# Kernel optimization log

Measured on AMD Instinct MI355X. Metric: run time of the kernel, lower is better.

Reference implementation:

```python
import jax, jax.numpy as jnp
import numpy as np

EPS = 1e-12  # matches torch F.normalize default eps
SCALE = 64.0  # fixed softmax temperature from the source

def _l2_normalize(x, axis):
    n = jnp.linalg.norm(x, ord=2, axis=axis, keepdims=True)
    return x / jnp.maximum(n, EPS)

def setup_inputs() -> dict:
    key = jax.random.key(0)
    k1, k2, k3 = jax.random.split(key, 3)
    B, L, S, D = 8, 2048, 2048, 128
    return {
        "query": jax.random.normal(k1, (B, L, D), dtype=jnp.float32),
        "key": jax.random.normal(k2, (B, S, D), dtype=jnp.float32),
        "value": jax.random.normal(k3, (B, S, D), dtype=jnp.float32),
    }

def reference(query, key, value):
    # rank-3 query path with norm=True, return_value=True, return_score=False
    q = _l2_normalize(query, axis=2)   # [B, L, D]
    k = _l2_normalize(key, axis=2)     # [B, S, D]
    score = jnp.einsum('nlk,nsk->nls', q, k)            # [B, L, S]
    score = jax.nn.softmax(score * SCALE, axis=2)
    # original does broadcast-multiply-then-sum; equivalent contraction:
    out = jnp.einsum('nls,nsd->nld', score, value)      # [B, L, D]
    return out
```

## Files before the change

### kernel.cpp

```cpp
#include <hip/hip_runtime.h>
#include <stdint.h>

#define Bb 8
#define Ll 2048
#define Ss 2048
#define Dd 128
#define NSB 4
#define SCHUNK 512
#define NROWS 16384
#define SCALE_LOG2E 92.33248261689366f

typedef __attribute__((ext_vector_type(8))) short bf16x8;
typedef __attribute__((ext_vector_type(16))) float f32x16;
typedef __attribute__((ext_vector_type(4))) unsigned u32x4;

__device__ __forceinline__ unsigned f2bf_pack(float a, float b) {
  unsigned ua = __float_as_uint(a); ua += 0x7fffu + ((ua >> 16) & 1u);
  unsigned ub = __float_as_uint(b); ub += 0x7fffu + ((ub >> 16) & 1u);
  return (ua >> 16) | (ub & 0xffff0000u);
}

__device__ __forceinline__ unsigned pkbf(float a, float b) {
#if __has_builtin(__builtin_amdgcn_cvt_pk_bf16_f32)
  auto r = __builtin_amdgcn_cvt_pk_bf16_f32(a, b);
  return __builtin_bit_cast(unsigned, r);
#else
  return f2bf_pack(a, b);
#endif
}

__device__ __forceinline__ void gl_lds16(const void* g, void* l) {
  __builtin_amdgcn_global_load_lds(
      (const __attribute__((address_space(1))) unsigned*)g,
      (__attribute__((address_space(3))) unsigned*)l, 16, 0, 0);
}

#define TRS 138
extern "C" __global__ __launch_bounds__(256)
void prep_kern(const float* __restrict__ Q, const float* __restrict__ K,
               const float* __restrict__ V,
               unsigned short* __restrict__ Qn, unsigned short* __restrict__ Kn,
               unsigned short* __restrict__ Vt) {
  __shared__ unsigned short T[32 * TRS];
  const int t = threadIdx.x;
  const int bid = blockIdx.x;
  if (bid < 8192) {
    const int lane = t & 63;
    int row = (bid << 2) + (t >> 6);
    int r = row;
    const float* src = Q; unsigned short* dst = Qn;
    if (row >= NROWS) { r = row - NROWS; src = K; dst = Kn; }
    float2 f = *(const float2*)(src + (size_t)r * Dd + lane * 2);
    float ss = f.x * f.x + f.y * f.y;
#pragma unroll
    for (int m = 1; m < 64; m <<= 1) ss += __shfl_xor(ss, m, 64);
    float inv = 1.0f / fmaxf(sqrtf(ss), 1e-12f);
    *(unsigned*)(dst + (size_t)r * Dd + lane * 2) = pkbf(f.x * inv, f.y * inv);
  } else {
    const int vb = bid - 8192;
    const int b = vb & 7, sw = vb >> 3;
    const int d4 = t & 31, sr = t >> 5;
#pragma unroll
    for (int p = 0; p < 4; ++p) {
      int sl = p * 8 + sr;
      float4 v = *(const float4*)(V + ((size_t)(b * Ss + sw * 32 + sl)) * Dd + d4 * 4);
      *(unsigned*)&T[sl * TRS + d4 * 4]     = pkbf(v.x, v.y);
      *(unsigned*)&T[sl * TRS + d4 * 4 + 2] = pkbf(v.z, v.w);
    }
    __syncthreads();
    const int so = t & 3, db = t >> 2;
#pragma unroll
    for (int p = 0; p < 2; ++p) {
      int d = p * 64 + db;
      unsigned u[4];
#pragma unroll
      for (int k = 0; k < 4; ++k) {
        unsigned lo = T[(so * 8 + 2 * k) * TRS + d];
        unsigned hi = T[(so * 8 + 2 * k + 1) * TRS + d];
        u[k] = lo | (hi << 16);
      }
      *(uint4*)(Vt + ((size_t)(b * Dd + d)) * Ss + sw * 32 + so * 8) =
          make_uint4(u[0], u[1], u[2], u[3]);
    }
  }
}

extern "C" __global__ __launch_bounds__(256, 2)
void attn_kern(const unsigned short* __restrict__ Qn,
               const unsigned short* __restrict__ Kn,
               const unsigned short* __restrict__ Vt,
               unsigned short* __restrict__ Op,
               float* __restrict__ Lp) {
  __shared__ unsigned short Kl[2][16 * 512];
  __shared__ unsigned short Vl[2][16 * 512];
  const int tid = threadIdx.x, wv = tid >> 6, lane = tid & 63;
  const int lm = lane & 31, h = lane >> 5;
  const int gid = blockIdx.x;
  const int grp = gid & 31, qt = gid >> 5;
  const int b = grp >> 2, sb = grp & 3;
  const int sbase = sb * SCHUNK;
  const int qrow = qt * 128 + wv * 32 + lm;

  const unsigned short* Qrow = Qn + ((size_t)(b * Ll + qrow)) * Dd;
  bf16x8 qf[8];
#pragma unroll
  for (int kt = 0; kt < 8; ++kt)
    qf[kt] = *(const bf16x8*)(Qrow + kt * 16 + h * 8);

  const unsigned short* Kb = Kn + (size_t)b * Ss * Dd;
  const unsigned short* Vb = Vt + (size_t)b * Dd * Ss;

  f32x16 o[4];
#pragma unroll
  for (int i = 0; i < 4; ++i)
#pragma unroll
    for (int r = 0; r < 16; ++r) o[i][r] = 0.f;

  auto stage = [&](int it, int buf) {
    const int s0 = sbase + it * 64;
#pragma unroll
    for (int i = 0; i < 4; ++i) {
      const int ks = wv * 4 + i;
      gl_lds16(Kb + (size_t)(s0 + (ks >> 3) * 32 + lm) * Dd + (ks & 7) * 16 + h * 8,
               &Kl[buf][ks * 512]);
    }
#pragma unroll
    for (int i = 0; i < 4; ++i) {
      const int vs = wv * 4 + i;
      gl_lds16(Vb + (size_t)((vs >> 2) * 32 + lm) * Ss + s0 + (vs & 3) * 16 + h * 8,
               &Vl[buf][vs * 512]);
    }
  };
  stage(0, 0);

  float lrun = 0.f;

#pragma unroll 1
  for (int it = 0; it < 8; ++it) {
    __syncthreads();
    const int cur = it & 1;
    if (it + 1 < 8) stage(it + 1, cur ^ 1);

    f32x16 st[2];
#pragma unroll
    for (int sblk = 0; sblk < 2; ++sblk) {
      f32x16 acc;
#pragma unroll
      for (int r = 0; r < 16; ++r) acc[r] = 0.f;
#pragma unroll
      for (int kt = 0; kt < 8; ++kt) {
        bf16x8 kf = *(const bf16x8*)&Kl[cur][(sblk * 8 + kt) * 512 + lane * 8];
        acc = __builtin_amdgcn_mfma_f32_32x32x16_bf16(kf, qf[kt], acc, 0, 0, 0);
      }
      st[sblk] = acc;
    }

    float ls = 0.f;
#pragma unroll
    for (int t = 0; t < 4; ++t) {
      float p[8];
#pragma unroll
      for (int j = 0; j < 8; ++j)
        p[j] = __builtin_amdgcn_exp2f(
            __builtin_fmaf(st[t >> 1][(t & 1) * 8 + j], SCALE_LOG2E, -SCALE_LOG2E));
      ls += ((p[0] + p[1]) + (p[2] + p[3])) + ((p[4] + p[5]) + (p[6] + p[7]));
      unsigned u0 = pkbf(p[0], p[1]), u1 = pkbf(p[2], p[3]);
      unsigned u2 = pkbf(p[4], p[5]), u3 = pkbf(p[6], p[7]);
      unsigned s0 = (unsigned)__shfl_xor((int)u0, 32, 64);
      unsigned s1 = (unsigned)__shfl_xor((int)u1, 32, 64);
      unsigned s2 = (unsigned)__shfl_xor((int)u2, 32, 64);
      unsigned s3 = (unsigned)__shfl_xor((int)u3, 32, 64);
      u32x4 fr;
      fr.x = h ? s2 : u0;
      fr.y = h ? s3 : u1;
      fr.z = h ? u2 : s0;
      fr.w = h ? u3 : s1;
      bf16x8 pf = __builtin_bit_cast(bf16x8, fr);
#pragma unroll
      for (int dblk = 0; dblk < 4; ++dblk) {
        bf16x8 vf = *(const bf16x8*)&Vl[cur][(dblk * 4 + t) * 512 + lane * 8];
        o[dblk] = __builtin_amdgcn_mfma_f32_32x32x16_bf16(vf, pf, o[dblk], 0, 0, 0);
      }
    }
    lrun += ls;
  }

  const float lt = lrun + __shfl_xor(lrun, 32, 64);
  unsigned short* Ob = Op + ((size_t)sb * NROWS + b * Ll + qrow) * Dd;
#pragma unroll
  for (int dblk = 0; dblk < 4; ++dblk)
#pragma unroll
    for (int g = 0; g < 4; ++g) {
      uint2 w;
      w.x = pkbf(o[dblk][g * 4 + 0], o[dblk][g * 4 + 1]);
      w.y = pkbf(o[dblk][g * 4 + 2], o[dblk][g * 4 + 3]);
      *(uint2*)(Ob + dblk * 32 + g * 8 + h * 4) = w;
    }
  if (h == 0) Lp[sb * NROWS + b * Ll + qrow] = lt;
}

extern "C" __global__ __launch_bounds__(256)
void comb_kern(const unsigned short* __restrict__ Op,
               const float* __restrict__ Lp, float* __restrict__ Out) {
  const int idx = blockIdx.x * 256 + threadIdx.x;
  const int row = idx >> 5;
  const int dof = (idx & 31) * 4;
  float den = 0.f;
#pragma unroll
  for (int s = 0; s < NSB; ++s) den += Lp[s * NROWS + row];
  float a0 = 0.f, a1 = 0.f, a2 = 0.f, a3 = 0.f;
#pragma unroll
  for (int s = 0; s < NSB; ++s) {
    uint2 v = *(const uint2*)(Op + ((size_t)s * NROWS + row) * Dd + dof);
    a0 += __uint_as_float(v.x << 16);
    a1 += __uint_as_float(v.x & 0xffff0000u);
    a2 += __uint_as_float(v.y << 16);
    a3 += __uint_as_float(v.y & 0xffff0000u);
  }
  const float inv = 1.f / den;
  float4 r; r.x = a0 * inv; r.y = a1 * inv; r.z = a2 * inv; r.w = a3 * inv;
  *(float4*)(Out + (size_t)row * Dd + dof) = r;
}

extern "C" void kernel_launch(void* const* d_in, const int* in_sizes, int n_in,
                              void* d_out, int out_size, void* d_ws, size_t ws_size,
                              hipStream_t stream) {
  const float* Q = (const float*)d_in[0];
  const float* K = (const float*)d_in[1];
  const float* V = (const float*)d_in[2];
  float* Out = (float*)d_out;
  unsigned short* Qn = (unsigned short*)d_ws;
  unsigned short* Kn = Qn + (size_t)NROWS * Dd;
  unsigned short* Vt = Kn + (size_t)NROWS * Dd;
  unsigned short* Op = Vt + (size_t)Bb * Dd * Ss;
  float* Lp = (float*)(Op + (size_t)NSB * NROWS * Dd);
  hipLaunchKernelGGL(prep_kern, dim3(8192 + 512), dim3(256), 0, stream, Q, K, V, Qn, Kn, Vt);
  hipLaunchKernelGGL(attn_kern, dim3(512), dim3(256), 0, stream, Qn, Kn, Vt, Op, Lp);
  hipLaunchKernelGGL(comb_kern, dim3(2048), dim3(256), 0, stream, Op, Lp, Out);
}
```

Before: 110.8 us.

## Split keys into eight chunks, load V directly to registers, shrink LDS

The key dimension is now split into eight 256-wide chunks instead of four, which doubles the attention grid to 1024 blocks. Each iteration now covers 32 keys instead of 64. V fragments are loaded straight from global memory into registers instead of being staged through LDS, so LDS holds only a double-buffered K tile and occupancy can rise to three blocks per CU. In exchange, the combine kernel must read twice as many bf16 partial outputs and the partial-output workspace doubles. The direct V loads are not covered by the pipeline, so their latency may be exposed.

After: 144.4 us. 1.3x slower.

```diff
diff --git a/kernel.cpp b/kernel.cpp
--- a/kernel.cpp
+++ b/kernel.cpp
@@ -5,8 +5,8 @@
 #define Ll 2048
 #define Ss 2048
 #define Dd 128
-#define NSB 4
-#define SCHUNK 512
+#define NSB 8
+#define SCHUNK 256
 #define NROWS 16384
 #define SCALE_LOG2E 92.33248261689366f
 
@@ -85,19 +85,18 @@
   }
 }
 
-extern "C" __global__ __launch_bounds__(256, 2)
+extern "C" __global__ __launch_bounds__(256, 3)
 void attn_kern(const unsigned short* __restrict__ Qn,
                const unsigned short* __restrict__ Kn,
                const unsigned short* __restrict__ Vt,
                unsigned short* __restrict__ Op,
                float* __restrict__ Lp) {
-  __shared__ unsigned short Kl[2][16 * 512];
-  __shared__ unsigned short Vl[2][16 * 512];
+  __shared__ unsigned short Kl[2][8 * 512];
   const int tid = threadIdx.x, wv = tid >> 6, lane = tid & 63;
   const int lm = lane & 31, h = lane >> 5;
   const int gid = blockIdx.x;
-  const int grp = gid & 31, qt = gid >> 5;
-  const int b = grp >> 2, sb = grp & 3;
+  const int grp = gid & 63, qt = gid >> 6;
+  const int b = grp >> 3, sb = grp & 7;
   const int sbase = sb * SCHUNK;
   const int qrow = qt * 128 + wv * 32 + lm;
 
@@ -116,22 +115,15 @@
 #pragma unroll
     for (int r = 0; r < 16; ++r) o[i][r] = 0.f;
 
-  auto stage = [&](int it, int buf) {
-    const int s0 = sbase + it * 64;
-#pragma unroll
-    for (int i = 0; i < 4; ++i) {
-      const int ks = wv * 4 + i;
-      gl_lds16(Kb + (size_t)(s0 + (ks >> 3) * 32 + lm) * Dd + (ks & 7) * 16 + h * 8,
-               &Kl[buf][ks * 512]);
-    }
-#pragma unroll
-    for (int i = 0; i < 4; ++i) {
-      const int vs = wv * 4 + i;
-      gl_lds16(Vb + (size_t)((vs >> 2) * 32 + lm) * Ss + s0 + (vs & 3) * 16 + h * 8,
-               &Vl[buf][vs * 512]);
+  auto stageK = [&](int it, int buf) {
+    const int s0 = sbase + it * 32;
+#pragma unroll
+    for (int i = 0; i < 2; ++i) {
+      const int kt = wv * 2 + i;
+      gl_lds16(Kb + (size_t)(s0 + lm) * Dd + kt * 16 + h * 8, &Kl[buf][kt * 512]);
     }
   };
-  stage(0, 0);
+  stageK(0, 0);
 
   float lrun = 0.f;
 
@@ -139,46 +131,49 @@
   for (int it = 0; it < 8; ++it) {
     __syncthreads();
     const int cur = it & 1;
-    if (it + 1 < 8) stage(it + 1, cur ^ 1);
-
-    f32x16 st[2];
-#pragma unroll
-    for (int sblk = 0; sblk < 2; ++sblk) {
-      f32x16 acc;
-#pragma unroll
-      for (int r = 0; r < 16; ++r) acc[r] = 0.f;
-#pragma unroll
-      for (int kt = 0; kt < 8; ++kt) {
-        bf16x8 kf = *(const bf16x8*)&Kl[cur][(sblk * 8 + kt) * 512 + lane * 8];
-        acc = __builtin_amdgcn_mfma_f32_32x32x16_bf16(kf, qf[kt], acc, 0, 0, 0);
-      }
-      st[sblk] = acc;
+    const int s0 = sbase + it * 32;
+    uint4 vfr[8];
+#pragma unroll
+    for (int dblk = 0; dblk < 4; ++dblk)
+#pragma unroll
+      for (int t = 0; t < 2; ++t)
+        vfr[dblk * 2 + t] =
+            *(const uint4*)(Vb + (size_t)(dblk * 32 + lm) * Ss + s0 + t * 16 + h * 8);
+    if (it + 1 < 8) stageK(it + 1, cur ^ 1);
+
+    f32x16 acc;
+#pragma unroll
+    for (int r = 0; r < 16; ++r) acc[r] = 0.f;
+#pragma unroll
+    for (int kt = 0; kt < 8; ++kt) {
+      bf16x8 kf = *(const bf16x8*)&Kl[cur][kt * 512 + lane * 8];
+      acc = __builtin_amdgcn_mfma_f32_32x32x16_bf16(kf, qf[kt], acc, 0, 0, 0);
     }
 
     float ls = 0.f;
 #pragma unroll
-    for (int t = 0; t < 4; ++t) {
+    for (int t = 0; t < 2; ++t) {
       float p[8];
 #pragma unroll
       for (int j = 0; j < 8; ++j)
         p[j] = __builtin_amdgcn_exp2f(
-            __builtin_fmaf(st[t >> 1][(t & 1) * 8 + j], SCALE_LOG2E, -SCALE_LOG2E));
+            __builtin_fmaf(acc[t * 8 + j], SCALE_LOG2E, -SCALE_LOG2E));
       ls += ((p[0] + p[1]) + (p[2] + p[3])) + ((p[4] + p[5]) + (p[6] + p[7]));
       unsigned u0 = pkbf(p[0], p[1]), u1 = pkbf(p[2], p[3]);
       unsigned u2 = pkbf(p[4], p[5]), u3 = pkbf(p[6], p[7]);
-      unsigned s0 = (unsigned)__shfl_xor((int)u0, 32, 64);
-      unsigned s1 = (unsigned)__shfl_xor((int)u1, 32, 64);
-      unsigned s2 = (unsigned)__shfl_xor((int)u2, 32, 64);
-      unsigned s3 = (unsigned)__shfl_xor((int)u3, 32, 64);
+      unsigned s0p = (unsigned)__shfl_xor((int)u0, 32, 64);
+      unsigned s1p = (unsigned)__shfl_xor((int)u1, 32, 64);
+      unsigned s2p = (unsigned)__shfl_xor((int)u2, 32, 64);
+      unsigned s3p = (unsigned)__shfl_xor((int)u3, 32, 64);
       u32x4 fr;
-      fr.x = h ? s2 : u0;
-      fr.y = h ? s3 : u1;
-      fr.z = h ? u2 : s0;
-      fr.w = h ? u3 : s1;
+      fr.x = h ? s2p : u0;
+      fr.y = h ? s3p : u1;
+      fr.z = h ? u2 : s0p;
+      fr.w = h ? u3 : s1p;
       bf16x8 pf = __builtin_bit_cast(bf16x8, fr);
 #pragma unroll
       for (int dblk = 0; dblk < 4; ++dblk) {
-        bf16x8 vf = *(const bf16x8*)&Vl[cur][(dblk * 4 + t) * 512 + lane * 8];
+        bf16x8 vf = __builtin_bit_cast(bf16x8, vfr[dblk * 2 + t]);
         o[dblk] = __builtin_amdgcn_mfma_f32_32x32x16_bf16(vf, pf, o[dblk], 0, 0, 0);
       }
     }
@@ -235,6 +230,6 @@
   unsigned short* Op = Vt + (size_t)Bb * Dd * Ss;
   float* Lp = (float*)(Op + (size_t)NSB * NROWS * Dd);
   hipLaunchKernelGGL(prep_kern, dim3(8192 + 512), dim3(256), 0, stream, Q, K, V, Qn, Kn, Vt);
-  hipLaunchKernelGGL(attn_kern, dim3(512), dim3(256), 0, stream, Qn, Kn, Vt, Op, Lp);
+  hipLaunchKernelGGL(attn_kern, dim3(1024), dim3(256), 0, stream, Qn, Kn, Vt, Op, Lp);
   hipLaunchKernelGGL(comb_kern, dim3(2048), dim3(256), 0, stream, Op, Lp, Out);
 }
```

## Pre-swizzle K and V into MFMA fragment order to remove shuffles

Applied to the files above, without the earlier changes.

The prep kernel now writes normalized K and transposed V directly in the per-lane MFMA fragment layout, as contiguous 4096-element tiles per 32-row block. The attention kernel then stages them with fully contiguous global-to-LDS loads. It also reorders V so the P fragment can be packed without cross-half-wave shuffles, and fuses the softmax/PV step into the QK loop. This aims to cut strided global loads and the ds_swizzle/select overhead, at the cost of a more complex prep kernel with an LDS round trip for K.

Measured after the change: 107.2 us. 1.03x faster.

```diff
diff --git a/kernel.cpp b/kernel.cpp
--- a/kernel.cpp
+++ b/kernel.cpp
@@ -12,7 +12,6 @@
 
 typedef __attribute__((ext_vector_type(8))) short bf16x8;
 typedef __attribute__((ext_vector_type(16))) float f32x16;
-typedef __attribute__((ext_vector_type(4))) unsigned u32x4;
 
 __device__ __forceinline__ unsigned f2bf_pack(float a, float b) {
   unsigned ua = __float_as_uint(a); ua += 0x7fffu + ((ua >> 16) & 1u);
@@ -35,60 +34,101 @@
       (__attribute__((address_space(3))) unsigned*)l, 16, 0, 0);
 }
 
-#define TRS 138
+
 extern "C" __global__ __launch_bounds__(256)
 void prep_kern(const float* __restrict__ Q, const float* __restrict__ K,
                const float* __restrict__ V,
-               unsigned short* __restrict__ Qn, unsigned short* __restrict__ Kn,
-               unsigned short* __restrict__ Vt) {
-  __shared__ unsigned short T[32 * TRS];
+               unsigned short* __restrict__ Qn, unsigned short* __restrict__ Kf,
+               unsigned short* __restrict__ Vf) {
+  __shared__ float Tf[32 * 130];
+  __shared__ float Ps[32 * 8];
+  __shared__ float Nr[32];
+  __shared__ unsigned short Tb[32 * 128];
   const int t = threadIdx.x;
   const int bid = blockIdx.x;
-  if (bid < 8192) {
+  if (bid < 4096) {
     const int lane = t & 63;
-    int row = (bid << 2) + (t >> 6);
-    int r = row;
-    const float* src = Q; unsigned short* dst = Qn;
-    if (row >= NROWS) { r = row - NROWS; src = K; dst = Kn; }
-    float2 f = *(const float2*)(src + (size_t)r * Dd + lane * 2);
+    const int r = bid * 4 + (t >> 6);
+    float2 f = *(const float2*)(Q + (size_t)r * Dd + lane * 2);
     float ss = f.x * f.x + f.y * f.y;
 #pragma unroll
     for (int m = 1; m < 64; m <<= 1) ss += __shfl_xor(ss, m, 64);
     float inv = 1.0f / fmaxf(sqrtf(ss), 1e-12f);
-    *(unsigned*)(dst + (size_t)r * Dd + lane * 2) = pkbf(f.x * inv, f.y * inv);
+    *(unsigned*)(Qn + (size_t)r * Dd + lane * 2) = pkbf(f.x * inv, f.y * inv);
+  } else if (bid < 4608) {
+    const int kb = bid - 4096;
+    const int b = kb & 7, sw = kb >> 3;
+    const int sl = t >> 3, d0 = (t & 7) * 16;
+    const float* src = K + ((size_t)(b * Ss + sw * 32 + sl)) * Dd + d0;
+    float ss = 0.f;
+#pragma unroll
+    for (int i = 0; i < 4; ++i) {
+      float4 v = *(const float4*)(src + i * 4);
+      Tf[sl * 130 + d0 + i * 4 + 0] = v.x;
+      Tf[sl * 130 + d0 + i * 4 + 1] = v.y;
+      Tf[sl * 130 + d0 + i * 4 + 2] = v.z;
+      Tf[sl * 130 + d0 + i * 4 + 3] = v.w;
+      ss += v.x * v.x + v.y * v.y + v.z * v.z + v.w * v.w;
+    }
+    Ps[sl * 8 + (t & 7)] = ss;
+    __syncthreads();
+    if (t < 32) {
+      float s = 0.f;
+#pragma unroll
+      for (int j = 0; j < 8; ++j) s += Ps[t * 8 + j];
+      Nr[t] = 1.0f / fmaxf(sqrtf(s), 1e-12f);
+    }
+    __syncthreads();
+    unsigned short* Ko = Kf + ((size_t)(b * 64 + sw)) * 4096;
+#pragma unroll
+    for (int p = 0; p < 2; ++p) {
+      const int run = p * 256 + t;
+      const int lane = run & 63, s = lane & 31, h = lane >> 5;
+      const int d = (run >> 6) * 16 + h * 8;
+      const float n = Nr[s];
+      const float* row = &Tf[s * 130 + d];
+      uint4 w;
+      w.x = pkbf(row[0] * n, row[1] * n);
+      w.y = pkbf(row[2] * n, row[3] * n);
+      w.z = pkbf(row[4] * n, row[5] * n);
+      w.w = pkbf(row[6] * n, row[7] * n);
+      *(uint4*)(Ko + run * 8) = w;
+    }
   } else {
-    const int vb = bid - 8192;
+    const int vb = bid - 4608;
     const int b = vb & 7, sw = vb >> 3;
-    const int d4 = t & 31, sr = t >> 5;
-#pragma unroll
-    for (int p = 0; p < 4; ++p) {
-      int sl = p * 8 + sr;
-      float4 v = *(const float4*)(V + ((size_t)(b * Ss + sw * 32 + sl)) * Dd + d4 * 4);
-      *(unsigned*)&T[sl * TRS + d4 * 4]     = pkbf(v.x, v.y);
-      *(unsigned*)&T[sl * TRS + d4 * 4 + 2] = pkbf(v.z, v.w);
-    }
-    __syncthreads();
-    const int so = t & 3, db = t >> 2;
+    const int sl = t >> 3, d0 = (t & 7) * 16;
+    const float* src = V + ((size_t)(b * Ss + sw * 32 + sl)) * Dd + d0;
+#pragma unroll
+    for (int i = 0; i < 4; ++i) {
+      float4 v = *(const float4*)(src + i * 4);
+      *(unsigned*)&Tb[sl * 128 + d0 + i * 4]     = pkbf(v.x, v.y);
+      *(unsigned*)&Tb[sl * 128 + d0 + i * 4 + 2] = pkbf(v.z, v.w);
+    }
+    __syncthreads();
+    unsigned short* Vo = Vf + ((size_t)(b * 64 + sw)) * 4096;
 #pragma unroll
     for (int p = 0; p < 2; ++p) {
-      int d = p * 64 + db;
-      unsigned u[4];
-#pragma unroll
-      for (int k = 0; k < 4; ++k) {
-        unsigned lo = T[(so * 8 + 2 * k) * TRS + d];
-        unsigned hi = T[(so * 8 + 2 * k + 1) * TRS + d];
-        u[k] = lo | (hi << 16);
+      const int run = p * 256 + t;
+      const int vslot = run >> 6, lane = run & 63;
+      const int dloc = lane & 31, h = lane >> 5;
+      const int dblk = vslot >> 1, t2 = vslot & 1;
+      const int d = dblk * 32 + dloc;
+      unsigned short w[8];
+#pragma unroll
+      for (int j = 0; j < 8; ++j) {
+        const int sloc = t2 * 16 + 4 * h + (j & 3) + 8 * (j >> 2);
+        w[j] = Tb[sloc * 128 + d];
       }
-      *(uint4*)(Vt + ((size_t)(b * Dd + d)) * Ss + sw * 32 + so * 8) =
-          make_uint4(u[0], u[1], u[2], u[3]);
+      *(uint4*)(Vo + run * 8) = *(uint4*)w;
     }
   }
 }
 
 extern "C" __global__ __launch_bounds__(256, 2)
 void attn_kern(const unsigned short* __restrict__ Qn,
-               const unsigned short* __restrict__ Kn,
-               const unsigned short* __restrict__ Vt,
+               const unsigned short* __restrict__ Kf,
+               const unsigned short* __restrict__ Vf,
                unsigned short* __restrict__ Op,
                float* __restrict__ Lp) {
   __shared__ unsigned short Kl[2][16 * 512];
@@ -96,9 +136,8 @@
   const int tid = threadIdx.x, wv = tid >> 6, lane = tid & 63;
   const int lm = lane & 31, h = lane >> 5;
   const int gid = blockIdx.x;
-  const int grp = gid & 31, qt = gid >> 5;
-  const int b = grp >> 2, sb = grp & 3;
-  const int sbase = sb * SCHUNK;
+  const int qt = gid >> 5, b = (gid >> 2) & 7, sb = gid & 3;
+  const int sblk0 = sb * (SCHUNK / 32);
   const int qrow = qt * 128 + wv * 32 + lm;
 
   const unsigned short* Qrow = Qn + ((size_t)(b * Ll + qrow)) * Dd;
@@ -107,8 +146,8 @@
   for (int kt = 0; kt < 8; ++kt)
     qf[kt] = *(const bf16x8*)(Qrow + kt * 16 + h * 8);
 
-  const unsigned short* Kb = Kn + (size_t)b * Ss * Dd;
-  const unsigned short* Vb = Vt + (size_t)b * Dd * Ss;
+  const unsigned short* Kc = Kf + ((size_t)(b * 64 + sblk0)) * 4096;
+  const unsigned short* Vc = Vf + ((size_t)(b * 64 + sblk0)) * 4096;
 
   f32x16 o[4];
 #pragma unroll
@@ -117,18 +156,13 @@
     for (int r = 0; r < 16; ++r) o[i][r] = 0.f;
 
   auto stage = [&](int it, int buf) {
-    const int s0 = sbase + it * 64;
 #pragma unroll
     for (int i = 0; i < 4; ++i) {
-      const int ks = wv * 4 + i;
-      gl_lds16(Kb + (size_t)(s0 + (ks >> 3) * 32 + lm) * Dd + (ks & 7) * 16 + h * 8,
-               &Kl[buf][ks * 512]);
-    }
-#pragma unroll
-    for (int i = 0; i < 4; ++i) {
-      const int vs = wv * 4 + i;
-      gl_lds16(Vb + (size_t)((vs >> 2) * 32 + lm) * Ss + s0 + (vs & 3) * 16 + h * 8,
-               &Vl[buf][vs * 512]);
+      const int sl = wv * 4 + i;
+      gl_lds16(Kc + (size_t)(it * 2 + (sl >> 3)) * 4096 + (sl & 7) * 512 + lane * 8,
+               &Kl[buf][sl * 512]);
+      gl_lds16(Vc + (size_t)(it * 2 + (sl >> 3)) * 4096 + (sl & 7) * 512 + lane * 8,
+               &Vl[buf][sl * 512]);
     }
   };
   stage(0, 0);
@@ -141,7 +175,6 @@
     const int cur = it & 1;
     if (it + 1 < 8) stage(it + 1, cur ^ 1);
 
-    f32x16 st[2];
 #pragma unroll
     for (int sblk = 0; sblk < 2; ++sblk) {
       f32x16 acc;
@@ -152,37 +185,28 @@
         bf16x8 kf = *(const bf16x8*)&Kl[cur][(sblk * 8 + kt) * 512 + lane * 8];
         acc = __builtin_amdgcn_mfma_f32_32x32x16_bf16(kf, qf[kt], acc, 0, 0, 0);
       }
-      st[sblk] = acc;
-    }
-
-    float ls = 0.f;
-#pragma unroll
-    for (int t = 0; t < 4; ++t) {
-      float p[8];
-#pragma unroll
-      for (int j = 0; j < 8; ++j)
-        p[j] = __builtin_amdgcn_exp2f(
-            __builtin_fmaf(st[t >> 1][(t & 1) * 8 + j], SCALE_LOG2E, -SCALE_LOG2E));
-      ls += ((p[0] + p[1]) + (p[2] + p[3])) + ((p[4] + p[5]) + (p[6] + p[7]));
-      unsigned u0 = pkbf(p[0], p[1]), u1 = pkbf(p[2], p[3]);
-      unsigned u2 = pkbf(p[4], p[5]), u3 = pkbf(p[6], p[7]);
-      unsigned s0 = (unsigned)__shfl_xor((int)u0, 32, 64);
-      unsigned s1 = (unsigned)__shfl_xor((int)u1, 32, 64);
-      unsigned s2 = (unsigned)__shfl_xor((int)u2, 32, 64);
-      unsigned s3 = (unsigned)__shfl_xor((int)u3, 32, 64);
-      u32x4 fr;
-      fr.x = h ? s2 : u0;
-      fr.y = h ? s3 : u1;
-      fr.z = h ? u2 : s0;
-      fr.w = h ? u3 : s1;
-      bf16x8 pf = __builtin_bit_cast(bf16x8, fr);
-#pragma unroll
-      for (int dblk = 0; dblk < 4; ++dblk) {
-        bf16x8 vf = *(const bf16x8*)&Vl[cur][(dblk * 4 + t) * 512 + lane * 8];
-        o[dblk] = __builtin_amdgcn_mfma_f32_32x32x16_bf16(vf, pf, o[dblk], 0, 0, 0);
+#pragma unroll
+      for (int t2 = 0; t2 < 2; ++t2) {
+        float p[8];
+#pragma unroll
+        for (int j = 0; j < 8; ++j)
+          p[j] = __builtin_amdgcn_exp2f(
+              __builtin_fmaf(acc[t2 * 8 + j], SCALE_LOG2E, -SCALE_LOG2E));
+        lrun += ((p[0] + p[1]) + (p[2] + p[3])) + ((p[4] + p[5]) + (p[6] + p[7]));
+        uint4 fr;
+        fr.x = pkbf(p[0], p[1]);
+        fr.y = pkbf(p[2], p[3]);
+        fr.z = pkbf(p[4], p[5]);
+        fr.w = pkbf(p[6], p[7]);
+        bf16x8 pf = __builtin_bit_cast(bf16x8, fr);
+#pragma unroll
+        for (int dblk = 0; dblk < 4; ++dblk) {
+          bf16x8 vf =
+              *(const bf16x8*)&Vl[cur][(sblk * 8 + dblk * 2 + t2) * 512 + lane * 8];
+          o[dblk] = __builtin_amdgcn_mfma_f32_32x32x16_bf16(vf, pf, o[dblk], 0, 0, 0);
+        }
       }
     }
-    lrun += ls;
   }
 
   const float lt = lrun + __shfl_xor(lrun, 32, 64);
@@ -230,11 +254,12 @@
   const float* V = (const float*)d_in[2];
   float* Out = (float*)d_out;
   unsigned short* Qn = (unsigned short*)d_ws;
-  unsigned short* Kn = Qn + (size_t)NROWS * Dd;
-  unsigned short* Vt = Kn + (size_t)NROWS * Dd;
-  unsigned short* Op = Vt + (size_t)Bb * Dd * Ss;
+  unsigned short* Kf = Qn + (size_t)NROWS * Dd;
+  unsigned short* Vf = Kf + (size_t)NROWS * Dd;
+  unsigned short* Op = Vf + (size_t)Bb * Dd * Ss;
   float* Lp = (float*)(Op + (size_t)NSB * NROWS * Dd);
-  hipLaunchKernelGGL(prep_kern, dim3(8192 + 512), dim3(256), 0, stream, Q, K, V, Qn, Kn, Vt);
-  hipLaunchKernelGGL(attn_kern, dim3(512), dim3(256), 0, stream, Qn, Kn, Vt, Op, Lp);
+  hipLaunchKernelGGL(prep_kern, dim3(4096 + 512 + 512), dim3(256), 0, stream,
+                     Q, K, V, Qn, Kf, Vf);
+  hipLaunchKernelGGL(attn_kern, dim3(512), dim3(256), 0, stream, Qn, Kf, Vf, Op, Lp);
   hipLaunchKernelGGL(comb_kern, dim3(2048), dim3(256), 0, stream, Op, Lp, Out);
 }
```
